# Kernel optimization log

Measured on AMD Instinct MI355X. Metric: run time of the kernel, lower is better.

## Reference

```python
import jax, jax.numpy as jnp
import numpy as np

B, T, H, UNITS = 64, 512, 1024, 1024

def setup_inputs() -> dict:
    key = jax.random.key(0)
    ks = jax.random.split(key, 8)
    s = 0.02
    return {
        "dec_hidden": jax.random.normal(ks[0], (B, H), jnp.float32),
        "enc_output": jax.random.normal(ks[1], (B, T, H), jnp.float32),
        "Wh": jax.random.normal(ks[2], (H, UNITS), jnp.float32) * s,
        "bh": jnp.zeros((UNITS,), jnp.float32),
        "Ws": jax.random.normal(ks[3], (H, UNITS), jnp.float32) * s,
        "bs": jnp.zeros((UNITS,), jnp.float32),
        "Wv": jax.random.normal(ks[4], (UNITS, 1), jnp.float32) * s,
        "bv": jnp.zeros((1,), jnp.float32),
    }

def reference(dec_hidden, enc_output, Wh, bh, Ws, bs, Wv, bv):
    # Faithful to original: tanh applied only to W_h(enc_output) term.
    enc_proj = jnp.tanh(jnp.einsum('bth,hu->btu', enc_output, Wh) + bh)  # [B,T,U]
    dec_proj = (dec_hidden @ Ws + bs)[:, None, :]                        # [B,1,U]
    score = jnp.einsum('btu,uo->bto', enc_proj + dec_proj, Wv) + bv      # [B,T,1]
    attn_dist = jax.nn.softmax(score, axis=1)                            # [B,T,1]
    context_vector = jnp.sum(attn_dist * enc_output, axis=1)             # [B,H]
    return context_vector, jnp.squeeze(attn_dist, axis=-1)
```

## Files before the change

### kernel.cpp

```cpp
#include <hip/hip_runtime.h>
#include <hip/hip_bf16.h>

typedef unsigned short u16;
typedef __attribute__((ext_vector_type(8))) short short8;
typedef __attribute__((ext_vector_type(4))) float f32x4;

#define B_  64
#define T_  512
#define H_  1024
#define U_  1024
#define BT_ (B_*T_)

#define BM 128
#define BN 128
#define BK 32

#define GLL16(gp, lp) __builtin_amdgcn_global_load_lds( \
    (const __attribute__((address_space(1))) void*)(gp), \
    (__attribute__((address_space(3))) void*)(lp), 16, 0, 0)

__device__ __forceinline__ u16 f32_to_bf16(float f) {
  union { float f; unsigned u; } v; v.f = f;
  unsigned r = v.u + 0x7FFFu + ((v.u >> 16) & 1u);
  return (u16)(r >> 16);
}
__device__ __forceinline__ unsigned pack_bf16x2(float lo, float hi) {
  return (unsigned)f32_to_bf16(lo) | ((unsigned)f32_to_bf16(hi) << 16);
}

__global__ __launch_bounds__(256) void ba_conv_enc(const float4* __restrict__ in,
                                                   uint4* __restrict__ out) {
  int i = blockIdx.x * 256 + threadIdx.x;
  float4 v0 = in[2 * i], v1 = in[2 * i + 1];
  uint4 o;
  o.x = pack_bf16x2(v0.x, v0.y);
  o.y = pack_bf16x2(v0.z, v0.w);
  o.z = pack_bf16x2(v1.x, v1.y);
  o.w = pack_bf16x2(v1.z, v1.w);
  out[i] = o;
}

__global__ __launch_bounds__(256) void ba_conv_whT(const float* __restrict__ wh,
                                                   u16* __restrict__ whT) {
  __shared__ float tile[32][33];
  int tx = threadIdx.x, ty = threadIdx.y;
  int u0 = blockIdx.x * 32, h0 = blockIdx.y * 32;
  #pragma unroll
  for (int i = 0; i < 32; i += 8)
    tile[ty + i][tx] = wh[(long)(h0 + ty + i) * U_ + u0 + tx];
  __syncthreads();
  #pragma unroll
  for (int i = 0; i < 32; i += 8)
    whT[(long)(u0 + ty + i) * H_ + h0 + tx] = f32_to_bf16(tile[tx][ty + i]);
}

__global__ __launch_bounds__(256, 4) void ba_score(
    const u16* __restrict__ A, const u16* __restrict__ Bt,
    const float* __restrict__ bh, const float* __restrict__ wv,
    float* __restrict__ score) {
  __shared__ u16 lA[BM * BK];
  __shared__ u16 lB[BN * BK];

  const int tid  = threadIdx.x;
  const int wid  = tid >> 6;
  const int lane = tid & 63;
  const int wm = wid >> 1, wn = wid & 1;
  const long row0  = (long)blockIdx.x * BM;
  const int  ncol0 = blockIdx.y * BN;

  const int c0 = 2 * wid, c1 = 2 * wid + 1;
  const int lsub = lane >> 2;
  const int csw = (((lane & 3) - ((lane >> 3) & 3)) & 3) * 8;

  const int fr = lane & 15;
  const int pofs = ((((lane >> 4) + ((lane >> 1) & 3)) & 3)) * 8;

  f32x4 acc[4][4];
  #pragma unroll
  for (int i = 0; i < 4; ++i)
    #pragma unroll
    for (int j = 0; j < 4; ++j) acc[i][j] = (f32x4){0.f, 0.f, 0.f, 0.f};

  for (int kt = 0; kt < H_; kt += BK) {
    GLL16(A + (row0 + 16 * c0 + lsub) * H_ + kt + csw, (char*)lA + c0 * 1024);
    GLL16(A + (row0 + 16 * c1 + lsub) * H_ + kt + csw, (char*)lA + c1 * 1024);
    GLL16(Bt + (long)(ncol0 + 16 * c0 + lsub) * H_ + kt + csw, (char*)lB + c0 * 1024);
    GLL16(Bt + (long)(ncol0 + 16 * c1 + lsub) * H_ + kt + csw, (char*)lB + c1 * 1024);
    __syncthreads();

    short8 av[4], bvv[4];
    #pragma unroll
    for (int i = 0; i < 4; ++i) {
      av[i]  = *(const short8*)&lA[(wm * 64 + i * 16 + fr) * BK + pofs];
      bvv[i] = *(const short8*)&lB[(wn * 64 + i * 16 + fr) * BK + pofs];
    }
    #pragma unroll
    for (int i = 0; i < 4; ++i)
      #pragma unroll
      for (int j = 0; j < 4; ++j)
        acc[i][j] = __builtin_amdgcn_mfma_f32_16x16x32_bf16(av[i], bvv[j], acc[i][j], 0, 0, 0);
    __syncthreads();
  }

  float sloc[4][4];
  #pragma unroll
  for (int i = 0; i < 4; ++i)
    #pragma unroll
    for (int r = 0; r < 4; ++r) sloc[i][r] = 0.f;

  #pragma unroll
  for (int j = 0; j < 4; ++j) {
    const int n = ncol0 + wn * 64 + j * 16 + fr;
    const float bhn = bh[n];
    const float wvn = wv[n];
    #pragma unroll
    for (int i = 0; i < 4; ++i) {
      #pragma unroll
      for (int r = 0; r < 4; ++r) {
        float x = acc[i][j][r] + bhn;
        float e = __expf(2.f * x);
        float t = 1.f - 2.f / (e + 1.f);
        sloc[i][r] += t * wvn;
      }
    }
  }

  #pragma unroll
  for (int i = 0; i < 4; ++i) {
    #pragma unroll
    for (int r = 0; r < 4; ++r) {
      float v = sloc[i][r];
      v += __shfl_xor(v, 1);
      v += __shfl_xor(v, 2);
      v += __shfl_xor(v, 4);
      v += __shfl_xor(v, 8);
      if ((lane & 15) == 0) {
        int m = wm * 64 + i * 16 + (lane >> 4) * 4 + r;
        atomicAdd(&score[row0 + m], v);
      }
    }
  }
}

__global__ __launch_bounds__(256) void ba_softmax(const float* __restrict__ score,
                                                  float* __restrict__ attn) {
  int b = blockIdx.x, tid = threadIdx.x;
  int lane = tid & 63, wid = tid >> 6;
  const float* s = score + b * T_;
  float v0 = s[tid], v1 = s[tid + 256];
  float m = fmaxf(v0, v1);
  #pragma unroll
  for (int o = 1; o < 64; o <<= 1) m = fmaxf(m, __shfl_xor(m, o));
  __shared__ float redm[4];
  __shared__ float reds[4];
  if (lane == 0) redm[wid] = m;
  __syncthreads();
  m = fmaxf(fmaxf(redm[0], redm[1]), fmaxf(redm[2], redm[3]));
  float e0 = __expf(v0 - m), e1 = __expf(v1 - m);
  float sum = e0 + e1;
  #pragma unroll
  for (int o = 1; o < 64; o <<= 1) sum += __shfl_xor(sum, o);
  if (lane == 0) reds[wid] = sum;
  __syncthreads();
  float tot = reds[0] + reds[1] + reds[2] + reds[3];
  float inv = 1.f / tot;
  attn[b * T_ + tid] = e0 * inv;
  attn[b * T_ + tid + 256] = e1 * inv;
}

__global__ __launch_bounds__(256) void ba_context(const float4* __restrict__ enc4,
                                                  const float* __restrict__ attn,
                                                  float* __restrict__ ctx) {
  int b = blockIdx.x;
  int t0 = blockIdx.y * 32;
  int tid = threadIdx.x;
  const float4* e = enc4 + ((long)b * T_ + t0) * (H_ / 4) + tid;
  const float* a = attn + b * T_ + t0;
  float4 acc = {0.f, 0.f, 0.f, 0.f};
  #pragma unroll 4
  for (int t = 0; t < 32; ++t) {
    float4 v = e[(long)t * (H_ / 4)];
    float at = a[t];
    acc.x = fmaf(at, v.x, acc.x);
    acc.y = fmaf(at, v.y, acc.y);
    acc.z = fmaf(at, v.z, acc.z);
    acc.w = fmaf(at, v.w, acc.w);
  }
  float* c = ctx + b * H_ + tid * 4;
  atomicAdd(c + 0, acc.x);
  atomicAdd(c + 1, acc.y);
  atomicAdd(c + 2, acc.z);
  atomicAdd(c + 3, acc.w);
}

extern "C" void kernel_launch(void* const* d_in, const int* in_sizes, int n_in,
                              void* d_out, int out_size, void* d_ws, size_t ws_size,
                              hipStream_t stream) {
  const float* enc = (const float*)d_in[1];
  const float* Wh  = (const float*)d_in[2];
  const float* bh  = (const float*)d_in[3];
  const float* Wv  = (const float*)d_in[6];

  float* out      = (float*)d_out;
  float* ctx_out  = out;
  float* attn_out = out + B_ * H_;

  char* ws = (char*)d_ws;
  u16*  encb   = (u16*)ws;
  u16*  whT    = (u16*)(ws + (size_t)67108864);
  float* score = (float*)(ws + (size_t)67108864 + 2097152);

  ba_conv_enc<<<BT_ * H_ / 8 / 256, 256, 0, stream>>>((const float4*)enc, (uint4*)encb);
  ba_conv_whT<<<dim3(U_ / 32, H_ / 32), dim3(32, 8), 0, stream>>>(Wh, whT);
  hipMemsetAsync(score, 0, BT_ * sizeof(float), stream);
  hipMemsetAsync(ctx_out, 0, B_ * H_ * sizeof(float), stream);
  ba_score<<<dim3(BT_ / BM, U_ / BN), 256, 0, stream>>>(encb, whT, bh, Wv, score);
  ba_softmax<<<B_, 256, 0, stream>>>(score, attn_out);
  ba_context<<<dim3(B_, 16), 256, 0, stream>>>((const float4*)enc, attn_out, ctx_out);
}
```

Baseline: 344.5 us.

## Double-buffer LDS tiles in score GEMM and replace context atomics with two-pass reduction

```diff
diff --git a/kernel.cpp b/kernel.cpp
--- a/kernel.cpp
+++ b/kernel.cpp
@@ -58,8 +58,8 @@
     const u16* __restrict__ A, const u16* __restrict__ Bt,
     const float* __restrict__ bh, const float* __restrict__ wv,
     float* __restrict__ score) {
-  __shared__ u16 lA[BM * BK];
-  __shared__ u16 lB[BN * BK];
+  __shared__ u16 lA[2][BM * BK];
+  __shared__ u16 lB[2][BN * BK];
 
   const int tid  = threadIdx.x;
   const int wid  = tid >> 6;
@@ -75,31 +75,47 @@
   const int fr = lane & 15;
   const int pofs = ((((lane >> 4) + ((lane >> 1) & 3)) & 3)) * 8;
 
+  const u16* gA0 = A + (row0 + 16 * c0 + lsub) * H_ + csw;
+  const u16* gA1 = A + (row0 + 16 * c1 + lsub) * H_ + csw;
+  const u16* gB0 = Bt + (long)(ncol0 + 16 * c0 + lsub) * H_ + csw;
+  const u16* gB1 = Bt + (long)(ncol0 + 16 * c1 + lsub) * H_ + csw;
+
   f32x4 acc[4][4];
   #pragma unroll
   for (int i = 0; i < 4; ++i)
     #pragma unroll
     for (int j = 0; j < 4; ++j) acc[i][j] = (f32x4){0.f, 0.f, 0.f, 0.f};
 
+  GLL16(gA0, (char*)lA[0] + c0 * 1024);
+  GLL16(gA1, (char*)lA[0] + c1 * 1024);
+  GLL16(gB0, (char*)lB[0] + c0 * 1024);
+  GLL16(gB1, (char*)lB[0] + c1 * 1024);
+  __syncthreads();
+
+  int cur = 0;
   for (int kt = 0; kt < H_; kt += BK) {
-    GLL16(A + (row0 + 16 * c0 + lsub) * H_ + kt + csw, (char*)lA + c0 * 1024);
-    GLL16(A + (row0 + 16 * c1 + lsub) * H_ + kt + csw, (char*)lA + c1 * 1024);
-    GLL16(Bt + (long)(ncol0 + 16 * c0 + lsub) * H_ + kt + csw, (char*)lB + c0 * 1024);
-    GLL16(Bt + (long)(ncol0 + 16 * c1 + lsub) * H_ + kt + csw, (char*)lB + c1 * 1024);
-    __syncthreads();
+    if (kt + BK < H_) {
+      const int nxt = cur ^ 1;
+      GLL16(gA0 + kt + BK, (char*)lA[nxt] + c0 * 1024);
+      GLL16(gA1 + kt + BK, (char*)lA[nxt] + c1 * 1024);
+      GLL16(gB0 + kt + BK, (char*)lB[nxt] + c0 * 1024);
+      GLL16(gB1 + kt + BK, (char*)lB[nxt] + c1 * 1024);
+    }
 
     short8 av[4], bvv[4];
     #pragma unroll
     for (int i = 0; i < 4; ++i) {
-      av[i]  = *(const short8*)&lA[(wm * 64 + i * 16 + fr) * BK + pofs];
-      bvv[i] = *(const short8*)&lB[(wn * 64 + i * 16 + fr) * BK + pofs];
+      av[i]  = *(const short8*)&lA[cur][(wm * 64 + i * 16 + fr) * BK + pofs];
+      bvv[i] = *(const short8*)&lB[cur][(wn * 64 + i * 16 + fr) * BK + pofs];
     }
     #pragma unroll
     for (int i = 0; i < 4; ++i)
       #pragma unroll
       for (int j = 0; j < 4; ++j)
         acc[i][j] = __builtin_amdgcn_mfma_f32_16x16x32_bf16(av[i], bvv[j], acc[i][j], 0, 0, 0);
+
     __syncthreads();
+    cur ^= 1;
   }
 
   float sloc[4][4];
@@ -168,14 +184,14 @@
   attn[b * T_ + tid + 256] = e1 * inv;
 }
 
-__global__ __launch_bounds__(256) void ba_context(const float4* __restrict__ enc4,
-                                                  const float* __restrict__ attn,
-                                                  float* __restrict__ ctx) {
+__global__ __launch_bounds__(256) void ba_context1(const float4* __restrict__ enc4,
+                                                   const float* __restrict__ attn,
+                                                   float4* __restrict__ part) {
   int b = blockIdx.x;
-  int t0 = blockIdx.y * 32;
+  int c = blockIdx.y;
   int tid = threadIdx.x;
-  const float4* e = enc4 + ((long)b * T_ + t0) * (H_ / 4) + tid;
-  const float* a = attn + b * T_ + t0;
+  const float4* e = enc4 + ((long)b * T_ + c * 32) * (H_ / 4) + tid;
+  const float* a = attn + b * T_ + c * 32;
   float4 acc = {0.f, 0.f, 0.f, 0.f};
   #pragma unroll 4
   for (int t = 0; t < 32; ++t) {
@@ -186,11 +202,21 @@
     acc.z = fmaf(at, v.z, acc.z);
     acc.w = fmaf(at, v.w, acc.w);
   }
-  float* c = ctx + b * H_ + tid * 4;
-  atomicAdd(c + 0, acc.x);
-  atomicAdd(c + 1, acc.y);
-  atomicAdd(c + 2, acc.z);
-  atomicAdd(c + 3, acc.w);
+  part[((long)b * 16 + c) * (H_ / 4) + tid] = acc;
+}
+
+__global__ __launch_bounds__(256) void ba_context2(const float4* __restrict__ part,
+                                                   float4* __restrict__ ctx) {
+  int b = blockIdx.x;
+  int tid = threadIdx.x;
+  const float4* p = part + (long)b * 16 * (H_ / 4) + tid;
+  float4 acc = {0.f, 0.f, 0.f, 0.f};
+  #pragma unroll
+  for (int c = 0; c < 16; ++c) {
+    float4 v = p[c * (H_ / 4)];
+    acc.x += v.x; acc.y += v.y; acc.z += v.z; acc.w += v.w;
+  }
+  ctx[b * (H_ / 4) + tid] = acc;
 }
 
 extern "C" void kernel_launch(void* const* d_in, const int* in_sizes, int n_in,
@@ -206,15 +232,16 @@
   float* attn_out = out + B_ * H_;
 
   char* ws = (char*)d_ws;
-  u16*  encb   = (u16*)ws;
-  u16*  whT    = (u16*)(ws + (size_t)67108864);
+  u16*   encb  = (u16*)ws;
+  u16*   whT   = (u16*)(ws + (size_t)67108864);
   float* score = (float*)(ws + (size_t)67108864 + 2097152);
+  float* part  = (float*)(ws + (size_t)67108864 + 2097152 + 131072);
 
   ba_conv_enc<<<BT_ * H_ / 8 / 256, 256, 0, stream>>>((const float4*)enc, (uint4*)encb);
   ba_conv_whT<<<dim3(U_ / 32, H_ / 32), dim3(32, 8), 0, stream>>>(Wh, whT);
   hipMemsetAsync(score, 0, BT_ * sizeof(float), stream);
-  hipMemsetAsync(ctx_out, 0, B_ * H_ * sizeof(float), stream);
   ba_score<<<dim3(BT_ / BM, U_ / BN), 256, 0, stream>>>(encb, whT, bh, Wv, score);
   ba_softmax<<<B_, 256, 0, stream>>>(score, attn_out);
-  ba_context<<<dim3(B_, 16), 256, 0, stream>>>((const float4*)enc, attn_out, ctx_out);
-}
+  ba_context1<<<dim3(B_, 16), 256, 0, stream>>>((const float4*)enc, attn_out, (float4*)part);
+  ba_context2<<<B_, 256, 0, stream>>>((const float4*)part, (float4*)ctx_out);
+}
```

Result: faster. 328.0 us (-4.8%).
